# Kernel tuning notes

Hardware: AMD Instinct MI355X
Metric: run time of the kernel (lower is better)

## Reference

```python
import jax, jax.numpy as jnp
import numpy as np

B, L = 2, 1024
DIM = 512
N_LAYERS = 2
D_STATE = 16
D_CONV = 4
D_INNER = 2 * DIM          # expand_factor=2
DT_RANK = (DIM + 15) // 16  # ceil(d_model/16) = 32
VOCAB = 32000


def _rmsnorm(x, w, eps=1e-5):
    return x * jax.lax.rsqrt(jnp.mean(x * x, axis=-1, keepdims=True) + eps) * w


def _causal_conv(x, w, b):
    # x: (B,L,D_INNER); depthwise causal conv along L, kernel D_CONV
    xt = jnp.transpose(x, (0, 2, 1))  # (B,C,L)
    y = jax.lax.conv_general_dilated(
        xt, w, window_strides=(1,), padding=[(D_CONV - 1, 0)],
        dimension_numbers=('NCH', 'OIH', 'NCH'), feature_group_count=D_INNER)
    return jnp.transpose(y, (0, 2, 1)) + b


def _ssm(x, xproj_w, dt_w, dt_b, A_log, Dp):
    # x: (B,L,D_INNER)
    A = -jnp.exp(A_log)  # (D_INNER, D_STATE)
    dbc = jnp.einsum('bld,rd->blr', x, xproj_w)  # (B,L,DT_RANK+2*D_STATE)
    delta = jax.nn.softplus(jnp.einsum('blr,dr->bld', dbc[..., :DT_RANK], dt_w) + dt_b)
    Bm = dbc[..., DT_RANK:DT_RANK + D_STATE]   # (B,L,D_STATE)
    Cm = dbc[..., DT_RANK + D_STATE:]          # (B,L,D_STATE)
    dA = jnp.exp(delta[..., None] * A)                       # (B,L,D_INNER,D_STATE)
    dBx = (delta * x)[..., None] * Bm[:, :, None, :]         # (B,L,D_INNER,D_STATE)

    def step(h, inp):
        a, b = inp
        h = a * h + b
        return h, h

    h0 = jnp.zeros((x.shape[0], D_INNER, D_STATE), x.dtype)
    _, hs = jax.lax.scan(step, h0, (jnp.swapaxes(dA, 0, 1), jnp.swapaxes(dBx, 0, 1)))
    y = jnp.einsum('lbds,bls->bld', hs, Cm) + Dp * x
    return y


def _block(h, rw, iw, cw, cb, xw, dw, db, Al, Dp, ow):
    r = _rmsnorm(h, rw)
    xz = jnp.einsum('bld,ed->ble', r, iw)  # (B,L,2*D_INNER)
    xin, z = jnp.split(xz, 2, axis=-1)
    xin = jax.nn.silu(_causal_conv(xin, cw, cb))
    y = _ssm(xin, xw, dw, db, Al, Dp) * jax.nn.silu(z)
    return h + jnp.einsum('ble,de->bld', y, ow)


def _forward(x, embed, rms_w, in_w, conv_w, conv_b, xproj_w, dt_w, dt_b, A_log, Dp, out_w, ln_g, ln_b, head_w, head_b):
    h = embed[x]  # (B,L,DIM)
    for l in range(N_LAYERS):
        h = _block(h, rms_w[l], in_w[l], conv_w[l], conv_b[l], xproj_w[l],
                   dt_w[l], dt_b[l], A_log[l], Dp[l], out_w[l])
    mu = jnp.mean(h, axis=-1, keepdims=True)
    var = jnp.mean((h - mu) ** 2, axis=-1, keepdims=True)
    hn = (h - mu) * jax.lax.rsqrt(var + 1e-5) * ln_g + ln_b
    return jnp.einsum('bld,vd->blv', hn, head_w) + head_b


def setup_inputs() -> dict:
    key = jax.random.key(0)
    ks = jax.random.split(key, 10)
    s = 0.02
    x = jax.random.randint(ks[0], (B, L), 0, VOCAB)
    embed = jax.random.normal(ks[1], (VOCAB, DIM), jnp.float32) * s
    rms_w = jnp.ones((N_LAYERS, DIM), jnp.float32)
    in_w = jax.random.normal(ks[2], (N_LAYERS, 2 * D_INNER, DIM), jnp.float32) * s
    conv_w = jax.random.normal(ks[3], (N_LAYERS, D_INNER, 1, D_CONV), jnp.float32) * s
    conv_b = jnp.zeros((N_LAYERS, D_INNER), jnp.float32)
    xproj_w = jax.random.normal(ks[4], (N_LAYERS, DT_RANK + 2 * D_STATE, D_INNER), jnp.float32) * s
    dt_w = jax.random.normal(ks[5], (N_LAYERS, D_INNER, DT_RANK), jnp.float32) * s
    dt_b = jax.random.normal(ks[6], (N_LAYERS, D_INNER), jnp.float32) * s
    A_log = jnp.log(jnp.broadcast_to(jnp.arange(1, D_STATE + 1, dtype=jnp.float32), (N_LAYERS, D_INNER, D_STATE)))
    Dp = jnp.ones((N_LAYERS, D_INNER), jnp.float32)
    out_w = jax.random.normal(ks[7], (N_LAYERS, DIM, D_INNER), jnp.float32) * s
    ln_g = jnp.ones((DIM,), jnp.float32)
    ln_b = jnp.zeros((DIM,), jnp.float32)
    head_w = jax.random.normal(ks[8], (VOCAB, DIM), jnp.float32) * s
    head_b = jnp.zeros((VOCAB,), jnp.float32)
    return dict(x=x, embed=embed, rms_w=rms_w, in_w=in_w, conv_w=conv_w, conv_b=conv_b,
                xproj_w=xproj_w, dt_w=dt_w, dt_b=dt_b, A_log=A_log, Dp=Dp, out_w=out_w,
                ln_g=ln_g, ln_b=ln_b, head_w=head_w, head_b=head_b)


def reference(x, embed, rms_w, in_w, conv_w, conv_b, xproj_w, dt_w, dt_b, A_log, Dp, out_w, ln_g, ln_b, head_w, head_b):
    return _forward(x, embed, rms_w, in_w, conv_w, conv_b, xproj_w, dt_w, dt_b,
                    A_log, Dp, out_w, ln_g, ln_b, head_w, head_b)
```

## Files before the change

### kernel.cpp

```cpp
#include <hip/hip_runtime.h>

typedef unsigned short u16;
typedef __attribute__((ext_vector_type(8))) __bf16 bf16x8;
typedef __attribute__((ext_vector_type(4))) float f32x4;

#define B_ 2
#define L_ 1024
#define DIM_ 512
#define DINNER_ 1024
#define DSTATE_ 16
#define DTRANK_ 32
#define VOCAB_ 32000
#define NCHUNK 64
#define CLEN 16

__device__ __forceinline__ u16 f2bf(float f) {
    union { float f; unsigned u; } x; x.f = f;
    unsigned r = x.u + 0x7FFFu + ((x.u >> 16) & 1u);
    return (u16)(r >> 16);
}

__global__ __launch_bounds__(256) void prep(const float* __restrict__ in_w,
                                            const float* __restrict__ out_w,
                                            const float* __restrict__ head_w,
                                            const float* __restrict__ dt_w,
                                            const int* __restrict__ x,
                                            const float* __restrict__ embed,
                                            const float* __restrict__ rw,
                                            u16* __restrict__ win,
                                            u16* __restrict__ wout,
                                            u16* __restrict__ whd,
                                            float* __restrict__ dtwT,
                                            float* __restrict__ h,
                                            u16* __restrict__ rbf) {
    int bk = blockIdx.x;
    int t = threadIdx.x;
    if (bk < 19072) {
        const int n1 = 524288;
        const int n2 = n1 + 262144;
        int i = bk * 256 + t;
        const float4* s; ushort4* d; int j;
        if (i < n1)      { s = (const float4*)in_w;   d = (ushort4*)win;  j = i; }
        else if (i < n2) { s = (const float4*)out_w;  d = (ushort4*)wout; j = i - n1; }
        else             { s = (const float4*)head_w; d = (ushort4*)whd;  j = i - n2; }
        float4 v = s[j];
        ushort4 o; o.x = f2bf(v.x); o.y = f2bf(v.y); o.z = f2bf(v.z); o.w = f2bf(v.w);
        d[j] = o;
    } else if (bk < 19328) {
        int bb = bk - 19072;
        int l = bb >> 7;
        int e = (bb & 127) * 256 + t;
        int r = e >> 10, d = e & 1023;
        dtwT[(size_t)l * 32768 + r * 1024 + d] = dt_w[(size_t)l * 32768 + d * 32 + r];
    } else {
        int wave = t >> 6, lane = t & 63;
        int row = (bk - 19328) * 4 + wave;
        int tok = x[row];
        const float4* s = (const float4*)(embed + (size_t)tok * DIM_);
        float4 v0 = s[lane], v1 = s[lane + 64];
        float4* hd = (float4*)(h + (size_t)row * DIM_);
        hd[lane] = v0;
        hd[lane + 64] = v1;
        float ss = v0.x*v0.x + v0.y*v0.y + v0.z*v0.z + v0.w*v0.w
                 + v1.x*v1.x + v1.y*v1.y + v1.z*v1.z + v1.w*v1.w;
        for (int m = 1; m < 64; m <<= 1) ss += __shfl_xor(ss, m);
        float rms = rsqrtf(ss * (1.0f / DIM_) + 1e-5f);
        const float4* w4 = (const float4*)rw;
        float4 w0 = w4[lane], w1 = w4[lane + 64];
        u16* o = rbf + (size_t)row * DIM_;
        ushort4 a, b;
        a.x = f2bf(v0.x * rms * w0.x); a.y = f2bf(v0.y * rms * w0.y);
        a.z = f2bf(v0.z * rms * w0.z); a.w = f2bf(v0.w * rms * w0.w);
        b.x = f2bf(v1.x * rms * w1.x); b.y = f2bf(v1.y * rms * w1.y);
        b.z = f2bf(v1.z * rms * w1.z); b.w = f2bf(v1.w * rms * w1.w);
        *(ushort4*)(o + lane * 4) = a;
        *(ushort4*)(o + 256 + lane * 4) = b;
    }
}

__global__ __launch_bounds__(256) void rmsnorm_bf16(const float* __restrict__ h,
                                                    const float* __restrict__ w,
                                                    u16* __restrict__ out) {
    int wave = threadIdx.x >> 6, lane = threadIdx.x & 63;
    int row = blockIdx.x * 4 + wave;
    const float4* r4 = (const float4*)(h + (size_t)row * DIM_);
    float4 v0 = r4[lane], v1 = r4[lane + 64];
    float ss = v0.x*v0.x + v0.y*v0.y + v0.z*v0.z + v0.w*v0.w
             + v1.x*v1.x + v1.y*v1.y + v1.z*v1.z + v1.w*v1.w;
    for (int m = 1; m < 64; m <<= 1) ss += __shfl_xor(ss, m);
    float rms = rsqrtf(ss * (1.0f / DIM_) + 1e-5f);
    const float4* w4 = (const float4*)w;
    float4 w0 = w4[lane], w1 = w4[lane + 64];
    u16* o = out + (size_t)row * DIM_;
    ushort4 a, b;
    a.x = f2bf(v0.x * rms * w0.x); a.y = f2bf(v0.y * rms * w0.y);
    a.z = f2bf(v0.z * rms * w0.z); a.w = f2bf(v0.w * rms * w0.w);
    b.x = f2bf(v1.x * rms * w1.x); b.y = f2bf(v1.y * rms * w1.y);
    b.z = f2bf(v1.z * rms * w1.z); b.w = f2bf(v1.w * rms * w1.w);
    *(ushort4*)(o + lane * 4) = a;
    *(ushort4*)(o + 256 + lane * 4) = b;
}

__global__ __launch_bounds__(256) void layernorm_bf16(const float* __restrict__ h,
                                                      const float* __restrict__ g,
                                                      const float* __restrict__ bta,
                                                      u16* __restrict__ out) {
    int wave = threadIdx.x >> 6, lane = threadIdx.x & 63;
    int row = blockIdx.x * 4 + wave;
    const float4* r4 = (const float4*)(h + (size_t)row * DIM_);
    float4 v0 = r4[lane], v1 = r4[lane + 64];
    float s = v0.x + v0.y + v0.z + v0.w + v1.x + v1.y + v1.z + v1.w;
    float ss = v0.x*v0.x + v0.y*v0.y + v0.z*v0.z + v0.w*v0.w
             + v1.x*v1.x + v1.y*v1.y + v1.z*v1.z + v1.w*v1.w;
    for (int m = 1; m < 64; m <<= 1) { s += __shfl_xor(s, m); ss += __shfl_xor(ss, m); }
    float mu = s * (1.0f / DIM_);
    float var = ss * (1.0f / DIM_) - mu * mu;
    float rs = rsqrtf(var + 1e-5f);
    const float4* g4 = (const float4*)g;
    const float4* b4 = (const float4*)bta;
    float4 g0 = g4[lane], g1 = g4[lane + 64];
    float4 b0 = b4[lane], b1 = b4[lane + 64];
    u16* o = out + (size_t)row * DIM_;
    ushort4 a, b;
    a.x = f2bf((v0.x - mu) * rs * g0.x + b0.x); a.y = f2bf((v0.y - mu) * rs * g0.y + b0.y);
    a.z = f2bf((v0.z - mu) * rs * g0.z + b0.z); a.w = f2bf((v0.w - mu) * rs * g0.w + b0.w);
    b.x = f2bf((v1.x - mu) * rs * g1.x + b1.x); b.y = f2bf((v1.y - mu) * rs * g1.y + b1.y);
    b.z = f2bf((v1.z - mu) * rs * g1.z + b1.z); b.w = f2bf((v1.w - mu) * rs * g1.w + b1.w);
    *(ushort4*)(o + lane * 4) = a;
    *(ushort4*)(o + 256 + lane * 4) = b;
}

template <int MODE>
__global__ __launch_bounds__(256) void gemm_bt(const u16* __restrict__ A,
                                               const u16* __restrict__ B,
                                               float* __restrict__ C,
                                               const float* __restrict__ bias,
                                               int M, int N, int K,
                                               int nbx, int swzq) {
    __shared__ u16 As[4][128 * 32];
    __shared__ u16 Bs[4][128 * 32];
    const int tid = threadIdx.x;
    const int wave = tid >> 6;
    const int lane = tid & 63;
    int lin = blockIdx.x;
    if (swzq) lin = (lin & 7) * swzq + (lin >> 3);
    const int m0 = (lin % nbx) * 128;
    const int n0 = (lin / nbx) * 128;
    const int wr = wave >> 1, wc = wave & 1;
    f32x4 acc[4][4] = {};

    const int sub = lane >> 2;
    const int slotL = lane & 3;
    const int fsub = (sub & 3) ^ ((sub >> 2) & 3);
    const int scol = (slotL ^ fsub) * 8;

    auto stage = [&](int buf, int kt) {
        int k0 = kt * 32;
        #pragma unroll
        for (int i = 0; i < 4; ++i) {
            int c = wave * 4 + i;
            const u16* src;
            u16* dst;
            if (c < 8) {
                int row = c * 16 + sub;
                src = A + (size_t)(m0 + row) * K + k0 + scol;
                dst = &As[buf][c * 512];
            } else {
                int cc = c - 8;
                int row = cc * 16 + sub;
                src = B + (size_t)(n0 + row) * K + k0 + scol;
                dst = &Bs[buf][cc * 512];
            }
            __builtin_amdgcn_global_load_lds((const __attribute__((address_space(1))) void*)src,
                                             (__attribute__((address_space(3))) void*)dst,
                                             16, 0, 0);
        }
    };

    const int nt = K / 32;
    stage(0, 0); stage(1, 1); stage(2, 2);

    const int fr = lane & 15;
    const int q = lane >> 4;
    const int fswz = (fr & 3) ^ ((fr >> 2) & 3);
    const int rdoff = ((q ^ fswz) * 8);

    for (int t = 0; t < nt; ++t) {
        if (t + 2 < nt)      asm volatile("s_waitcnt vmcnt(8)" ::: "memory");
        else if (t + 1 < nt) asm volatile("s_waitcnt vmcnt(4)" ::: "memory");
        else                 asm volatile("s_waitcnt vmcnt(0)" ::: "memory");
        __builtin_amdgcn_sched_barrier(0);
        __builtin_amdgcn_s_barrier();
        asm volatile("" ::: "memory");
        __builtin_amdgcn_sched_barrier(0);
        if (t + 3 < nt) stage((t + 3) & 3, t + 3);
        const u16* Ab = &As[t & 3][0];
        const u16* Bb = &Bs[t & 3][0];
        bf16x8 a[4], b[4];
        #pragma unroll
        for (int mi = 0; mi < 4; ++mi)
            a[mi] = *(const bf16x8*)(Ab + (wr * 64 + mi * 16 + fr) * 32 + rdoff);
        #pragma unroll
        for (int ni = 0; ni < 4; ++ni)
            b[ni] = *(const bf16x8*)(Bb + (wc * 64 + ni * 16 + fr) * 32 + rdoff);
        __builtin_amdgcn_s_setprio(1);
        #pragma unroll
        for (int mi = 0; mi < 4; ++mi)
            #pragma unroll
            for (int ni = 0; ni < 4; ++ni)
                acc[mi][ni] = __builtin_amdgcn_mfma_f32_16x16x32_bf16(a[mi], b[ni], acc[mi][ni], 0, 0, 0);
        __builtin_amdgcn_s_setprio(0);
    }

    const int cl = lane & 15;
    const int rq = (lane >> 4) * 4;
    #pragma unroll
    for (int mi = 0; mi < 4; ++mi) {
        #pragma unroll
        for (int ni = 0; ni < 4; ++ni) {
            int col = n0 + wc * 64 + ni * 16 + cl;
            #pragma unroll
            for (int rr = 0; rr < 4; ++rr) {
                int row = m0 + wr * 64 + mi * 16 + rq + rr;
                size_t idx = (size_t)row * N + col;
                float v = acc[mi][ni][rr];
                if (MODE == 2)      C[idx] = v + bias[col];
                else                C[idx] = v;
            }
        }
    }
}

template <int MODE>
__global__ __launch_bounds__(256) void gemm64(const u16* __restrict__ A,
                                              const u16* __restrict__ B,
                                              float* __restrict__ C,
                                              int M, int N, int K,
                                              int nbx, int swzq) {
    __shared__ u16 As[4][64 * 64];
    __shared__ u16 Bs[4][64 * 64];
    const int tid = threadIdx.x;
    const int wave = tid >> 6;
    const int lane = tid & 63;
    int lin = blockIdx.x;
    if (swzq) lin = (lin & 7) * swzq + (lin >> 3);
    const int m0 = (lin % nbx) * 64;
    const int n0 = (lin / nbx) * 64;
    const int wr = wave >> 1, wc = wave & 1;
    f32x4 acc[2][2] = {};

    const int crow = lane >> 3;
    const int scol = ((lane & 7) ^ crow) * 8;

    auto stage = [&](int buf, int kt) {
        int k0 = kt * 64;
        #pragma unroll
        for (int i = 0; i < 4; ++i) {
            int c = wave * 4 + i;
            const u16* src;
            u16* dst;
            if (c < 8) {
                int row = c * 8 + crow;
                src = A + (size_t)(m0 + row) * K + k0 + scol;
                dst = &As[buf][c * 512];
            } else {
                int cc = c - 8;
                int row = cc * 8 + crow;
                src = B + (size_t)(n0 + row) * K + k0 + scol;
                dst = &Bs[buf][cc * 512];
            }
            __builtin_amdgcn_global_load_lds((const __attribute__((address_space(1))) void*)src,
                                             (__attribute__((address_space(3))) void*)dst,
                                             16, 0, 0);
        }
    };

    const int nt = K / 64;
    stage(0, 0); stage(1, 1); stage(2, 2);

    const int fr = lane & 15;
    const int q = lane >> 4;

    for (int t = 0; t < nt; ++t) {
        if (t + 2 < nt)      asm volatile("s_waitcnt vmcnt(8)" ::: "memory");
        else if (t + 1 < nt) asm volatile("s_waitcnt vmcnt(4)" ::: "memory");
        else                 asm volatile("s_waitcnt vmcnt(0)" ::: "memory");
        __builtin_amdgcn_sched_barrier(0);
        __builtin_amdgcn_s_barrier();
        asm volatile("" ::: "memory");
        __builtin_amdgcn_sched_barrier(0);
        if (t + 3 < nt) stage((t + 3) & 3, t + 3);
        const u16* Ab = &As[t & 3][0];
        const u16* Bb = &Bs[t & 3][0];
        bf16x8 a[2][2], b[2][2];
        #pragma unroll
        for (int ki = 0; ki < 2; ++ki) {
            #pragma unroll
            for (int mi = 0; mi < 2; ++mi) {
                int row = wr * 32 + mi * 16 + fr;
                a[ki][mi] = *(const bf16x8*)(Ab + row * 64 + ((((ki << 2) + q) ^ (fr & 7)) * 8));
            }
            #pragma unroll
            for (int ni = 0; ni < 2; ++ni) {
                int row = wc * 32 + ni * 16 + fr;
                b[ki][ni] = *(const bf16x8*)(Bb + row * 64 + ((((ki << 2) + q) ^ (fr & 7)) * 8));
            }
        }
        __builtin_amdgcn_s_setprio(1);
        #pragma unroll
        for (int ki = 0; ki < 2; ++ki)
            #pragma unroll
            for (int mi = 0; mi < 2; ++mi)
                #pragma unroll
                for (int ni = 0; ni < 2; ++ni)
                    acc[mi][ni] = __builtin_amdgcn_mfma_f32_16x16x32_bf16(a[ki][mi], b[ki][ni], acc[mi][ni], 0, 0, 0);
        __builtin_amdgcn_s_setprio(0);
    }

    const int cl = lane & 15;
    const int rq = (lane >> 4) * 4;
    #pragma unroll
    for (int mi = 0; mi < 2; ++mi) {
        #pragma unroll
        for (int ni = 0; ni < 2; ++ni) {
            int col = n0 + wc * 32 + ni * 16 + cl;
            #pragma unroll
            for (int rr = 0; rr < 4; ++rr) {
                int row = m0 + wr * 32 + mi * 16 + rq + rr;
                size_t idx = (size_t)row * N + col;
                float v = acc[mi][ni][rr];
                if (MODE == 1)      C[idx] += v;
                else                C[idx] = v;
            }
        }
    }
}

__global__ __launch_bounds__(256) void conv_xproj_dt(const float* __restrict__ xz,
                                                     const float* __restrict__ cw,
                                                     const float* __restrict__ cb,
                                                     const float* __restrict__ xw,
                                                     const float* __restrict__ dtwT,
                                                     const float* __restrict__ dtb,
                                                     float* __restrict__ xc,
                                                     float* __restrict__ dbc,
                                                     float* __restrict__ delta) {
    __shared__ float sxc[8 * 1024];
    __shared__ float sxw[64 * 132];
    __shared__ float sred[4][8][68];
    __shared__ float sdbc[8][64];
    int t = threadIdx.x;
    int m0 = blockIdx.x * 8;
    #pragma unroll
    for (int i = 0; i < 32; ++i) {
        int idx = t + i * 256;
        int mi = idx >> 10, d = idx & 1023;
        int m = m0 + mi;
        int l = m & (L_ - 1);
        float acc = cb[d];
        #pragma unroll
        for (int j = 0; j < 4; ++j) {
            int ll = l - 3 + j;
            if (ll >= 0) acc = fmaf(cw[d * 4 + j], xz[(size_t)(m - 3 + j) * (2 * DINNER_) + d], acc);
        }
        float sv = acc / (1.0f + __expf(-acc));
        sxc[mi * 1024 + d] = sv;
        xc[(size_t)m * DINNER_ + d] = sv;
    }
    const int n = t & 63, kg = t >> 6;
    float acc8[8] = {};
    for (int kc = 0; kc < 8; ++kc) {
        __syncthreads();
        #pragma unroll
        for (int i = 0; i < 8; ++i) {
            int f = t + i * 256;
            int row = f >> 5, col4 = f & 31;
            *(float4*)(&sxw[row * 132 + col4 * 4]) =
                *(const float4*)(xw + (size_t)row * DINNER_ + kc * 128 + col4 * 4);
        }
        __syncthreads();
        #pragma unroll
        for (int k4i = 0; k4i < 8; ++k4i) {
            int k4 = kg * 8 + k4i;
            float4 wv = *(const float4*)(&sxw[n * 132 + k4 * 4]);
            #pragma unroll
            for (int mi = 0; mi < 8; ++mi) {
                float4 xv = *(const float4*)(&sxc[mi * 1024 + kc * 128 + k4 * 4]);
                acc8[mi] += wv.x * xv.x + wv.y * xv.y + wv.z * xv.z + wv.w * xv.w;
            }
        }
    }
    #pragma unroll
    for (int mi = 0; mi < 8; ++mi) sred[kg][mi][n] = acc8[mi];
    __syncthreads();
    #pragma unroll
    for (int rep = 0; rep < 2; ++rep) {
        int o = t + rep * 256;
        int mi = o >> 6, n2 = o & 63;
        float v = sred[0][mi][n2] + sred[1][mi][n2] + sred[2][mi][n2] + sred[3][mi][n2];
        sdbc[mi][n2] = v;
        dbc[(size_t)(m0 + mi) * 64 + n2] = v;
    }
    __syncthreads();
    {
        int d0 = t * 4;
        float4 bias = *(const float4*)(dtb + d0);
        float4 am[8];
        #pragma unroll
        for (int mi = 0; mi < 8; ++mi) am[mi] = bias;
        const float4* wT = (const float4*)dtwT;
        #pragma unroll
        for (int r = 0; r < 32; ++r) {
            float4 wv = wT[r * 256 + t];
            #pragma unroll
            for (int mi = 0; mi < 8; ++mi) {
                float s = sdbc[mi][r];
                am[mi].x = fmaf(s, wv.x, am[mi].x);
                am[mi].y = fmaf(s, wv.y, am[mi].y);
                am[mi].z = fmaf(s, wv.z, am[mi].z);
                am[mi].w = fmaf(s, wv.w, am[mi].w);
            }
        }
        #pragma unroll
        for (int mi = 0; mi < 8; ++mi) {
            float4 o;
            o.x = (am[mi].x > 20.f) ? am[mi].x : log1pf(__expf(am[mi].x));
            o.y = (am[mi].y > 20.f) ? am[mi].y : log1pf(__expf(am[mi].y));
            o.z = (am[mi].z > 20.f) ? am[mi].z : log1pf(__expf(am[mi].z));
            o.w = (am[mi].w > 20.f) ? am[mi].w : log1pf(__expf(am[mi].w));
            *(float4*)(delta + (size_t)(m0 + mi) * DINNER_ + d0) = o;
        }
    }
}

__global__ __launch_bounds__(256) void ssm_part1(const float* __restrict__ delta,
                                                 const float* __restrict__ xc,
                                                 const float* __restrict__ dbc,
                                                 const float* __restrict__ A_log,
                                                 float* __restrict__ hfin,
                                                 float* __restrict__ sumd) {
    int tid = threadIdx.x;
    int d = blockIdx.x * 256 + tid;
    int c = blockIdx.y;
    int b = blockIdx.z;
    __shared__ float sB[CLEN][DSTATE_];
    {
        int l = tid >> 4, s = tid & 15;
        sB[l][s] = dbc[((size_t)(b * L_ + c * CLEN + l)) * 64 + DTRANK_ + s];
    }
    float A[16], h[16];
    {
        const float4* Ar = (const float4*)(A_log + (size_t)d * DSTATE_);
        #pragma unroll
        for (int i = 0; i < 4; ++i) {
            float4 al = Ar[i];
            A[i * 4 + 0] = -__expf(al.x); A[i * 4 + 1] = -__expf(al.y);
            A[i * 4 + 2] = -__expf(al.z); A[i * 4 + 3] = -__expf(al.w);
        }
    }
    #pragma unroll
    for (int s = 0; s < 16; ++s) h[s] = 0.f;
    __syncthreads();
    float sd = 0.f;
    size_t base = ((size_t)b * L_ + c * CLEN) * DINNER_ + d;
    #pragma unroll
    for (int l = 0; l < CLEN; ++l) {
        float dv = delta[base + (size_t)l * DINNER_];
        float xv = xc[base + (size_t)l * DINNER_];
        sd += dv;
        float dx = dv * xv;
        #pragma unroll
        for (int s = 0; s < 16; ++s) {
            float e = __expf(dv * A[s]);
            h[s] = fmaf(e, h[s], dx * sB[l][s]);
        }
    }
    float* hf = hfin + (((size_t)b * NCHUNK + c) * DINNER_ + d) * 16;
    #pragma unroll
    for (int i = 0; i < 4; ++i) {
        float4 v; v.x = h[i*4]; v.y = h[i*4+1]; v.z = h[i*4+2]; v.w = h[i*4+3];
        *(float4*)(hf + i * 4) = v;
    }
    sumd[((size_t)b * NCHUNK + c) * DINNER_ + d] = sd;
}

__global__ __launch_bounds__(256) void ssm_carry(const float* __restrict__ hfin,
                                                 const float* __restrict__ sumd,
                                                 const float* __restrict__ A_log,
                                                 float* __restrict__ h0buf) {
    int t = blockIdx.x * 256 + threadIdx.x;
    int s = t & 15;
    int dg = t >> 4;
    int d = dg & (DINNER_ - 1);
    int b = dg >> 10;
    float As = -__expf(A_log[(size_t)d * DSTATE_ + s]);
    float hc = 0.f;
    #pragma unroll 4
    for (int c = 0; c < NCHUNK; ++c) {
        size_t k = (((size_t)b * NCHUNK + c) * DINNER_ + d) * 16 + s;
        h0buf[k] = hc;
        float sdv = sumd[((size_t)b * NCHUNK + c) * DINNER_ + d];
        float hf = hfin[k];
        hc = fmaf(__expf(As * sdv), hc, hf);
    }
}

__global__ __launch_bounds__(256) void ssm_part2(const float* __restrict__ delta,
                                                 const float* __restrict__ xc,
                                                 const float* __restrict__ dbc,
                                                 const float* __restrict__ xz,
                                                 const float* __restrict__ A_log,
                                                 const float* __restrict__ Dp,
                                                 const float* __restrict__ h0buf,
                                                 u16* __restrict__ ys) {
    int tid = threadIdx.x;
    int d = blockIdx.x * 256 + tid;
    int c = blockIdx.y;
    int b = blockIdx.z;
    __shared__ float sBC[CLEN][32];
    {
        int l = tid >> 5, j = tid & 31;
        sBC[l][j] = dbc[((size_t)(b * L_ + c * CLEN + l)) * 64 + DTRANK_ + j];
        int e1 = tid + 256;
        l = e1 >> 5; j = e1 & 31;
        sBC[l][j] = dbc[((size_t)(b * L_ + c * CLEN + l)) * 64 + DTRANK_ + j];
    }
    float A[16], h[16];
    {
        const float4* Ar = (const float4*)(A_log + (size_t)d * DSTATE_);
        #pragma unroll
        for (int i = 0; i < 4; ++i) {
            float4 al = Ar[i];
            A[i * 4 + 0] = -__expf(al.x); A[i * 4 + 1] = -__expf(al.y);
            A[i * 4 + 2] = -__expf(al.z); A[i * 4 + 3] = -__expf(al.w);
        }
        const float4* h0 = (const float4*)(h0buf + (((size_t)b * NCHUNK + c) * DINNER_ + d) * 16);
        #pragma unroll
        for (int i = 0; i < 4; ++i) {
            float4 v = h0[i];
            h[i * 4 + 0] = v.x; h[i * 4 + 1] = v.y; h[i * 4 + 2] = v.z; h[i * 4 + 3] = v.w;
        }
    }
    float Dval = Dp[d];
    __syncthreads();
    size_t base = ((size_t)b * L_ + c * CLEN) * DINNER_ + d;
    size_t zbase = ((size_t)b * L_ + c * CLEN) * (2 * DINNER_) + DINNER_ + d;
    #pragma unroll
    for (int l = 0; l < CLEN; ++l) {
        float dv = delta[base + (size_t)l * DINNER_];
        float xv = xc[base + (size_t)l * DINNER_];
        float zv = xz[zbase + (size_t)l * (2 * DINNER_)];
        float dx = dv * xv;
        float y = 0.f;
        #pragma unroll
        for (int s = 0; s < 16; ++s) {
            float e = __expf(dv * A[s]);
            h[s] = fmaf(e, h[s], dx * sBC[l][s]);
            y = fmaf(h[s], sBC[l][16 + s], y);
        }
        y = fmaf(Dval, xv, y);
        float sg = zv / (1.0f + __expf(-zv));
        ys[base + (size_t)l * DINNER_] = f2bf(y * sg);
    }
}

extern "C" void kernel_launch(void* const* d_in, const int* in_sizes, int n_in,
                              void* d_out, int out_size, void* d_ws, size_t ws_size,
                              hipStream_t stream) {
    const int*   x       = (const int*)d_in[0];
    const float* embed   = (const float*)d_in[1];
    const float* rms_w   = (const float*)d_in[2];
    const float* in_w    = (const float*)d_in[3];
    const float* conv_w  = (const float*)d_in[4];
    const float* conv_b  = (const float*)d_in[5];
    const float* xproj_w = (const float*)d_in[6];
    const float* dt_w    = (const float*)d_in[7];
    const float* dt_b    = (const float*)d_in[8];
    const float* A_log   = (const float*)d_in[9];
    const float* Dp      = (const float*)d_in[10];
    const float* out_w   = (const float*)d_in[11];
    const float* ln_g    = (const float*)d_in[12];
    const float* ln_b    = (const float*)d_in[13];
    const float* head_w  = (const float*)d_in[14];
    const float* head_b  = (const float*)d_in[15];
    float* out = (float*)d_out;

    char* p = (char*)d_ws;
    auto take = [&](size_t n) { char* q = p; p += (n + 255) & ~(size_t)255; return q; };
    float* h    = (float*)take(2048ull * 512 * 4);
    u16*   r_bf = (u16*)  take(2048ull * 512 * 2);
    float* xz   = (float*)take(2048ull * 2048 * 4);
    float* xc   = (float*)take(2048ull * 1024 * 4);
    float* dbc  = (float*)take(2048ull * 64 * 4);
    float* dlt  = (float*)take(2048ull * 1024 * 4);
    u16*   ys   = (u16*)  take(2048ull * 1024 * 2);
    u16*   hn   = (u16*)  take(2048ull * 512 * 2);
    u16*   win  = (u16*)  take(2ull * 2048 * 512 * 2);
    u16*   wout = (u16*)  take(2ull * 512 * 1024 * 2);
    u16*   whd  = (u16*)  take(32000ull * 512 * 2);
    float* dtwT = (float*)take(2ull * 32 * 1024 * 4);
    float* hfin = (float*)take((size_t)B_ * NCHUNK * DINNER_ * 16 * 4);
    float* h0b  = (float*)take((size_t)B_ * NCHUNK * DINNER_ * 16 * 4);
    float* sumd = (float*)take((size_t)B_ * NCHUNK * DINNER_ * 4);

    prep<<<19840, 256, 0, stream>>>(in_w, out_w, head_w, dt_w, x, embed, rms_w,
                                    win, wout, whd, dtwT, h, r_bf);

    for (int l = 0; l < 2; ++l) {
        if (l > 0) rmsnorm_bf16<<<512, 256, 0, stream>>>(h, rms_w + l * DIM_, r_bf);
        gemm_bt<0><<<256, 256, 0, stream>>>(r_bf, win + (size_t)l * 2048 * 512, xz, nullptr, 2048, 2048, 512, 16, 32);
        conv_xproj_dt<<<256, 256, 0, stream>>>(xz, conv_w + l * DINNER_ * 4, conv_b + l * DINNER_,
                                               xproj_w + (size_t)l * 64 * 1024,
                                               dtwT + (size_t)l * 32 * 1024, dt_b + l * DINNER_,
                                               xc, dbc, dlt);
        ssm_part1<<<dim3(4, NCHUNK, B_), 256, 0, stream>>>(dlt, xc, dbc, A_log + (size_t)l * DINNER_ * DSTATE_, hfin, sumd);
        ssm_carry<<<128, 256, 0, stream>>>(hfin, sumd, A_log + (size_t)l * DINNER_ * DSTATE_, h0b);
        ssm_part2<<<dim3(4, NCHUNK, B_), 256, 0, stream>>>(dlt, xc, dbc, xz, A_log + (size_t)l * DINNER_ * DSTATE_,
                                                           Dp + l * DINNER_, h0b, ys);
        gemm64<1><<<256, 256, 0, stream>>>(ys, wout + (size_t)l * 512 * 1024, h, 2048, 512, 1024, 32, 32);
    }

    layernorm_bf16<<<512, 256, 0, stream>>>(h, ln_g, ln_b, hn);
    gemm_bt<2><<<4000, 256, 0, stream>>>(hn, whd, out, head_b, 2048, VOCAB_, 512, 16, 500);
}
```

Baseline: 373.9 us.

## Add 256x256-tile pipelined MFMA GEMM for the vocabulary head projection

Replaces the 128x128-tile head GEMM with a new 512-thread kernel computing 256x256 output tiles. Operands are staged through a 4-deep LDS ring filled by direct global-to-LDS loads with an XOR swizzle, and explicit vmcnt waits keep several K-slices in flight. The larger tile is meant to raise arithmetic intensity and cut redundant operand loads. In exchange it uses a large LDS footprint limiting occupancy to one block per CU, and launches only 1000 blocks, which may leave a tail imbalance across CUs.

Result: faster. 361.7 us (-3.3%).

```diff
diff --git a/kernel.cpp b/kernel.cpp
--- a/kernel.cpp
+++ b/kernel.cpp
@@ -231,6 +231,105 @@
     }
 }
 
+__global__ __launch_bounds__(512) void gemm256(const u16* __restrict__ A,
+                                               const u16* __restrict__ B,
+                                               float* __restrict__ C,
+                                               const float* __restrict__ bias,
+                                               int M, int N, int K,
+                                               int nbx, int swzq) {
+    __shared__ u16 As[4][256 * 32];
+    __shared__ u16 Bs[4][256 * 32];
+    const int tid = threadIdx.x;
+    const int wave = tid >> 6;
+    const int lane = tid & 63;
+    int lin = blockIdx.x;
+    if (swzq) lin = (lin & 7) * swzq + (lin >> 3);
+    const int m0 = (lin % nbx) * 256;
+    const int n0 = (lin / nbx) * 256;
+    const int wrM = wave >> 2;
+    const int wcN = wave & 3;
+    f32x4 acc[8][4] = {};
+
+    const int sub = lane >> 2;
+    const int slotL = lane & 3;
+    const int fsub = (sub & 3) ^ ((sub >> 2) & 3);
+    const int scol = (slotL ^ fsub) * 8;
+
+    auto stage = [&](int buf, int kt) {
+        int k0 = kt * 32;
+        #pragma unroll
+        for (int i = 0; i < 4; ++i) {
+            int c = wave * 4 + i;
+            const u16* src;
+            u16* dst;
+            if (c < 16) {
+                int row = c * 16 + sub;
+                src = A + (size_t)(m0 + row) * K + k0 + scol;
+                dst = &As[buf][c * 512];
+            } else {
+                int cc = c - 16;
+                int row = cc * 16 + sub;
+                src = B + (size_t)(n0 + row) * K + k0 + scol;
+                dst = &Bs[buf][cc * 512];
+            }
+            __builtin_amdgcn_global_load_lds((const __attribute__((address_space(1))) void*)src,
+                                             (__attribute__((address_space(3))) void*)dst,
+                                             16, 0, 0);
+        }
+    };
+
+    const int nt = K / 32;
+    stage(0, 0); stage(1, 1); stage(2, 2);
+
+    const int fr = lane & 15;
+    const int q = lane >> 4;
+    const int fswz = (fr & 3) ^ ((fr >> 2) & 3);
+    const int rdoff = ((q ^ fswz) * 8);
+
+    for (int t = 0; t < nt; ++t) {
+        if (t + 2 < nt)      asm volatile("s_waitcnt vmcnt(8)" ::: "memory");
+        else if (t + 1 < nt) asm volatile("s_waitcnt vmcnt(4)" ::: "memory");
+        else                 asm volatile("s_waitcnt vmcnt(0)" ::: "memory");
+        __builtin_amdgcn_sched_barrier(0);
+        __builtin_amdgcn_s_barrier();
+        asm volatile("" ::: "memory");
+        __builtin_amdgcn_sched_barrier(0);
+        if (t + 3 < nt) stage((t + 3) & 3, t + 3);
+        const u16* Ab = &As[t & 3][0];
+        const u16* Bb = &Bs[t & 3][0];
+        bf16x8 a[8], b[4];
+        #pragma unroll
+        for (int mi = 0; mi < 8; ++mi)
+            a[mi] = *(const bf16x8*)(Ab + (wrM * 128 + mi * 16 + fr) * 32 + rdoff);
+        #pragma unroll
+        for (int ni = 0; ni < 4; ++ni)
+            b[ni] = *(const bf16x8*)(Bb + (wcN * 64 + ni * 16 + fr) * 32 + rdoff);
+        __builtin_amdgcn_s_setprio(1);
+        #pragma unroll
+        for (int mi = 0; mi < 8; ++mi)
+            #pragma unroll
+            for (int ni = 0; ni < 4; ++ni)
+                acc[mi][ni] = __builtin_amdgcn_mfma_f32_16x16x32_bf16(a[mi], b[ni], acc[mi][ni], 0, 0, 0);
+        __builtin_amdgcn_s_setprio(0);
+    }
+
+    const int cl = lane & 15;
+    const int rq = (lane >> 4) * 4;
+    #pragma unroll
+    for (int mi = 0; mi < 8; ++mi) {
+        #pragma unroll
+        for (int ni = 0; ni < 4; ++ni) {
+            int col = n0 + wcN * 64 + ni * 16 + cl;
+            float bv = bias[col];
+            #pragma unroll
+            for (int rr = 0; rr < 4; ++rr) {
+                int row = m0 + wrM * 128 + mi * 16 + rq + rr;
+                C[(size_t)row * N + col] = acc[mi][ni][rr] + bv;
+            }
+        }
+    }
+}
+
 template <int MODE>
 __global__ __launch_bounds__(256) void gemm64(const u16* __restrict__ A,
                                               const u16* __restrict__ B,
@@ -621,5 +720,5 @@
     }
 
     layernorm_bf16<<<512, 256, 0, stream>>>(h, ln_g, ln_b, hn);
-    gemm_bt<2><<<4000, 256, 0, stream>>>(hn, whd, out, head_b, 2048, VOCAB_, 512, 16, 500);
-}
+    gemm256<<<1000, 512, 0, stream>>>(hn, whd, out, head_b, 2048, VOCAB_, 512, 8, 125);
+}
```
